# Performance work log

Measured on AMD Instinct MI355X. Metric: run time of the kernel, lower is better.

## Reference

```python
import jax, jax.numpy as jnp
import numpy as np
from jax import lax

# 4th-order Butterworth lowpass, scipy.signal.butter(4, 0.2)
B_COEF = np.array([0.004824343357716228, 0.019297373430864913, 0.02894606014629737,
                   0.019297373430864913, 0.004824343357716228], dtype=np.float32)
A_COEF = np.array([1.0, -2.369513007182038, 2.3139884144006453,
                   -1.0546654058785672, 0.18737949236818502], dtype=np.float32)


def setup_inputs() -> dict:
    key = jax.random.key(0)
    x = jax.random.normal(key, (8, 64, 48000), dtype=jnp.float32)
    return {"x": x, "b": jnp.asarray(B_COEF), "a": jnp.asarray(A_COEF)}


def _pad_odd(x, n):
    # Faithful to torch _pad_odd (including its exact slicing on the right side).
    left = 2.0 * x[..., 0:1] - jnp.flip(x[..., 0:n], axis=-1)
    right = 2.0 * x[..., -1:] - jnp.flip(x[..., -(n + 2):-2], axis=-1)
    return jnp.concatenate([left, x, right], axis=-1)


def _lfilter(x, a, b):
    # y[n] = (sum_k b[k] x[n-k] - sum_j a[j] y[n-j]) / a[0]
    a0 = a[0]
    bn = b / a0
    an = a[1:] / a0                      # [N], N = order
    ntaps = b.shape[0]                   # static
    N = a.shape[0] - 1                   # static
    T = x.shape[-1]
    # FIR part: small static tap loop, fully vectorized over batch/time.
    pad = [(0, 0)] * (x.ndim - 1) + [(ntaps - 1, 0)]
    xp = jnp.pad(x, pad)
    f = bn[0] * xp[..., ntaps - 1: ntaps - 1 + T]
    for k in range(1, ntaps):
        f = f + bn[k] * xp[..., ntaps - 1 - k: ntaps - 1 - k + T]
    # IIR recurrence via scan over time.
    f_t = jnp.moveaxis(f, -1, 0)         # [T, B, C]
    init = jnp.zeros(x.shape[:-1] + (N,), x.dtype)  # [B, C, N], y[t-1..t-N]

    def step(carry, ft):
        y = ft - jnp.einsum('k,...k->...', an, carry)
        carry = jnp.concatenate([y[..., None], carry[..., :-1]], axis=-1)
        return carry, y

    _, ys = lax.scan(step, init, f_t)
    return jnp.moveaxis(ys, 0, -1)       # [B, C, T]


def _filtfilt(x, a, b):
    y = _lfilter(x, a, b)
    return jnp.flip(_lfilter(jnp.flip(y, axis=-1), a, b), axis=-1)


def reference(x, b, a):
    scale = jnp.max(jnp.abs(x), axis=-1, keepdims=True)
    xs = x / scale
    padlen = 3 * max(int(a.shape[0]), int(b.shape[0]))  # 15, static
    xp = _pad_odd(xs, padlen)
    y = _filtfilt(xp, a, b)
    y = y[..., padlen:-padlen]
    return y * scale
```

## Files before the change

kernel.cpp:

```cpp
#include <hip/hip_runtime.h>


#define T48 48000
#define TP0 48030
#define LCH 48
#define NCH 1024
#define UF  8192

#define BAR_LDS() do { \
  asm volatile("s_waitcnt lgkmcnt(0)" ::: "memory"); \
  __builtin_amdgcn_s_barrier(); \
} while (0)

__device__ __forceinline__ float fget(const float4& v, int e) {
  switch (e & 3) { case 0: return v.x; case 1: return v.y; case 2: return v.z; default: return v.w; }
}

#define MAPPLY(t, M, q) do { \
  (t).x += (M)[0]*(q).x  + (M)[1]*(q).y  + (M)[2]*(q).z  + (M)[3]*(q).w; \
  (t).y += (M)[4]*(q).x  + (M)[5]*(q).y  + (M)[6]*(q).z  + (M)[7]*(q).w; \
  (t).z += (M)[8]*(q).x  + (M)[9]*(q).y  + (M)[10]*(q).z + (M)[11]*(q).w; \
  (t).w += (M)[12]*(q).x + (M)[13]*(q).y + (M)[14]*(q).z + (M)[15]*(q).w; \
} while (0)

__global__ __launch_bounds__(1024, 4) void filtfilt_k(
    const float* __restrict__ x, const float* __restrict__ bco,
    const float* __restrict__ aco, float* __restrict__ out)
{
  __shared__ __align__(16) float U[UF];
  __shared__ float P[3][16];

  const int c = threadIdx.x;
  const float* __restrict__ xs = x + (size_t)blockIdx.x * T48;
  const float4* __restrict__ xs4 = reinterpret_cast<const float4*>(xs);
  float* __restrict__ os = out + (size_t)blockIdx.x * T48;
  float4* __restrict__ os4 = reinterpret_cast<float4*>(os);
  float4* __restrict__ U4 = reinterpret_cast<float4*>(U);

  const float inva0 = 1.f / aco[0];
  const float b0 = bco[0]*inva0, b1 = bco[1]*inva0, b2 = bco[2]*inva0,
              b3 = bco[3]*inva0, b4 = bco[4]*inva0;
  const float na1 = -aco[1]*inva0, na2 = -aco[2]*inva0,
              na3 = -aco[3]*inva0, na4 = -aco[4]*inva0;

  float4 F[14];
  const int fb = 12*c - 5;
#pragma unroll
  for (int k = 0; k < 14; k++) {
    int m = min(max(fb + k, 0), 11999);
    F[k] = xs4[m];
  }

  if (c < 64) {
    const int i = (c >> 2) & 3, j = c & 3;
    float r1 = (j==0)?1.f:0.f, r2 = (j==1)?1.f:0.f,
          r3 = (j==2)?1.f:0.f, r4 = (j==3)?1.f:0.f;
#pragma unroll
    for (int n = 0; n < LCH; n++) {
      float h = fmaf(na1, r1, fmaf(na2, r2, fmaf(na3, r3, na4 * r4)));
      r4 = r3; r3 = r2; r2 = r1; r1 = h;
    }
    float c0 = __shfl(r1, j), c1 = __shfl(r2, j),
          c2 = __shfl(r3, j), c3 = __shfl(r4, j);
    float Pv = (i==0)?c0 : (i==1)?c1 : (i==2)?c2 : c3;
    if (c < 16) P[0][c] = Pv;
    const float P0v = Pv;
    {
      float rA0 = __shfl(Pv, i*4+0), rA1 = __shfl(Pv, i*4+1),
            rA2 = __shfl(Pv, i*4+2), rA3 = __shfl(Pv, i*4+3);
      float cB0 = __shfl(Pv, 0*4+j), cB1 = __shfl(Pv, 1*4+j),
            cB2 = __shfl(Pv, 2*4+j), cB3 = __shfl(Pv, 3*4+j);
      Pv = rA0*cB0 + rA1*cB1 + rA2*cB2 + rA3*cB3;
    }
    if (c < 16) P[1][c] = Pv;
    {
      float rA0 = __shfl(Pv, i*4+0), rA1 = __shfl(Pv, i*4+1),
            rA2 = __shfl(Pv, i*4+2), rA3 = __shfl(Pv, i*4+3);
      float cB0 = __shfl(P0v, 0*4+j), cB1 = __shfl(P0v, 1*4+j),
            cB2 = __shfl(P0v, 2*4+j), cB3 = __shfl(P0v, 3*4+j);
      Pv = rA0*cB0 + rA1*cB1 + rA2*cB2 + rA3*cB3;
    }
    if (c < 16) P[2][c] = Pv;
  }

  float w4v = F[0].y, w3v = F[0].z, w2v = F[0].w, w1v = F[1].x;
  float A[LCH];
#pragma unroll
  for (int n = 0; n < LCH; n++) A[n] = fget(F[(n + 5) >> 2], (n + 5) & 3);

  if (c == 0) {
    float x0d = 2.f * xs[0];
    w4v = 0.f; w3v = 0.f; w2v = 0.f; w1v = 0.f;
#pragma unroll
    for (int n = 0; n < 15; n++) A[n] = x0d - xs[14 - n];
  }
  if (c >= 1000) {
    float xld = 2.f * xs[T48 - 1];
#define RFIX(p, var) do { int _p = (p); \
    if (_p >= 48015) var = (_p < TP0) ? (xld - xs[96012 - _p]) : 0.f; } while (0)
    RFIX(48*c - 4, w4v); RFIX(48*c - 3, w3v);
    RFIX(48*c - 2, w2v); RFIX(48*c - 1, w1v);
#pragma unroll
    for (int n = 0; n < LCH; n++) {
      int p = 48*c + n;
      if (p >= 48015) A[n] = (p < TP0) ? (xld - xs[96012 - p]) : 0.f;
    }
#undef RFIX
  }

  BAR_LDS();

  float r1 = 0.f, r2 = 0.f, r3 = 0.f, r4 = 0.f;
#pragma unroll
  for (int n = 0; n < LCH; n++) {
    float xv = A[n];
    float f = fmaf(b0,xv, fmaf(b1,w1v, fmaf(b2,w2v, fmaf(b3,w3v, b4*w4v))));
    w4v = w3v; w3v = w2v; w2v = w1v; w1v = xv;
    float u = fmaf(na4, r4, f);
    u = fmaf(na3, r3, u); u = fmaf(na2, r2, u); u = fmaf(na1, r1, u);
    A[n] = u; r4 = r3; r3 = r2; r2 = r1; r1 = u;
  }

  float4* Sb0 = U4;
  float4* Sb1 = U4 + 1024;
  Sb0[c] = make_float4(r1, r2, r3, r4);
  BAR_LDS();
  float4 sv = make_float4(0.f,0.f,0.f,0.f);
  if (c > 0) {
    sv = Sb0[c-1];
    if (c > 1) { float4 q = Sb0[c-2]; MAPPLY(sv, P[0], q); }
    if (c > 2) { float4 q = Sb0[c-3]; MAPPLY(sv, P[1], q); }
    if (c > 3) { float4 q = Sb0[c-4]; MAPPLY(sv, P[2], q); }
  }

  {
    float h1 = sv.x, h2 = sv.y, h3 = sv.z, h4 = sv.w;
#pragma unroll
    for (int n = 0; n < LCH; n++) {
      float h = fmaf(na1, h1, fmaf(na2, h2, fmaf(na3, h3, na4 * h4)));
      A[n] += h;
      h4 = h3; h3 = h2; h2 = h1; h1 = h;
    }
  }
  if (c >= 1000) {
#pragma unroll
    for (int n = 0; n < LCH; n++) if (48*c + n >= TP0) A[n] = 0.f;
  }

  Sb1[c] = make_float4(A[0], A[1], A[2], A[3]);
  BAR_LDS();
  float h0 = 0.f, h1v = 0.f, h2v = 0.f, h3v = 0.f;
  if (c < NCH - 1) { float4 hv = Sb1[c+1]; h0 = hv.x; h1v = hv.y; h2v = hv.z; h3v = hv.w; }

#define YV(i) ((i) < 48 ? A[(i)] : ((i)==48 ? h0 : (i)==49 ? h1v : (i)==50 ? h2v : h3v))
  r1 = 0.f; r2 = 0.f; r3 = 0.f; r4 = 0.f;
#pragma unroll
  for (int m = 0; m < LCH; m++) {
    float g = fmaf(b0, YV(47-m), fmaf(b1, YV(48-m),
              fmaf(b2, YV(49-m), fmaf(b3, YV(50-m), b4 * YV(51-m)))));
    float u = fmaf(na4, r4, g);
    u = fmaf(na3, r3, u); u = fmaf(na2, r2, u); u = fmaf(na1, r1, u);
    r4 = r3; r3 = r2; r2 = r1; r1 = u;
    if      (m == 0) h3v = u;
    else if (m == 1) h2v = u;
    else if (m == 2) h1v = u;
    else if (m == 3) h0  = u;
    else             A[51 - m] = u;
  }
#undef YV

  const int d = NCH - 1 - c;
  Sb0[d] = make_float4(r1, r2, r3, r4);
  BAR_LDS();
  float4 ev = make_float4(0.f,0.f,0.f,0.f);
  if (d > 0) {
    ev = Sb0[d-1];
    if (d > 1) { float4 q = Sb0[d-2]; MAPPLY(ev, P[0], q); }
    if (d > 2) { float4 q = Sb0[d-3]; MAPPLY(ev, P[1], q); }
    if (d > 3) { float4 q = Sb0[d-4]; MAPPLY(ev, P[2], q); }
  }

  {
    float g1 = ev.x, g2 = ev.y, g3 = ev.z, g4 = ev.w;
#pragma unroll
    for (int m = 0; m < LCH; m++) {
      float h = fmaf(na1, g1, fmaf(na2, g2, fmaf(na3, g3, na4 * g4)));
      if      (m == 0) h3v += h;
      else if (m == 1) h2v += h;
      else if (m == 2) h1v += h;
      else if (m == 3) h0  += h;
      else             A[51 - m] += h;
      g4 = g3; g3 = g2; g2 = g1; g1 = h;
    }
  }

  {
    const int base = 48*c - 15;
    if (base >= 0 && base < T48 - 2) {
      os[base+0] = A[4]; os[base+1] = A[5]; os[base+2] = A[6];
    }
#pragma unroll
    for (int k = 0; k < 10; k++) {
      int t4 = 12*c - 3 + k;
      if (t4 >= 0 && t4 < 12000)
        os4[t4] = make_float4(A[7+4*k], A[8+4*k], A[9+4*k], A[10+4*k]);
    }
    {
      int t4 = 12*c + 7;
      if (t4 < 12000) os4[t4] = make_float4(A[47], h0, h1v, h2v);
    }
    {
      int t = 48*c + 32;
      if (t < T48) os[t] = h3v;
    }
  }
}

extern "C" void kernel_launch(void* const* d_in, const int* in_sizes, int n_in,
                              void* d_out, int out_size, void* d_ws, size_t ws_size,
                              hipStream_t stream) {
  (void)n_in; (void)d_ws; (void)ws_size; (void)out_size;
  const float* x = (const float*)d_in[0];
  const float* b = (const float*)d_in[1];
  const float* a = (const float*)d_in[2];
  float* out = (float*)d_out;
  const int nseq = in_sizes[0] / T48;
  filtfilt_k<<<dim3(nseq), dim3(1024), 0, stream>>>(x, b, a, out);
}
```

Baseline: 219.7 us.

## Split each sequence across four 256-thread blocks using truncated state propagation

Each sequence now goes to four 256-thread blocks instead of one 1024-thread block. Each block covers 251 output chunks plus two halo chunks, and the halo absorbs the chunk carry-ins. The inter-chunk state prefix is cut to two neighbour terms, dropping the precomputed P^2 and P^3 matrices, on the premise that the filter's impulse response decays to negligible size after about 96 samples. Output is staged through shared memory so each thread writes 12 aligned float4s, which removes the scalar and edge stores. This raises the block count and shrinks barrier scope, but it repeats the halo work and is only approximately exact because the recurrence is truncated.

New measurement: 199.1 us. -9.4%, faster.

```diff
diff --git a/kernel.cpp b/kernel.cpp
--- a/kernel.cpp
+++ b/kernel.cpp
@@ -4,8 +4,7 @@
 #define T48 48000
 #define TP0 48030
 #define LCH 48
-#define NCH 1024
-#define UF  8192
+#define NOUT 251
 
 #define BAR_LDS() do { \
   asm volatile("s_waitcnt lgkmcnt(0)" ::: "memory"); \
@@ -23,19 +22,21 @@
   (t).w += (M)[12]*(q).x + (M)[13]*(q).y + (M)[14]*(q).z + (M)[15]*(q).w; \
 } while (0)
 
-__global__ __launch_bounds__(1024, 4) void filtfilt_k(
+__global__ __launch_bounds__(256, 4) void filtfilt_k(
     const float* __restrict__ x, const float* __restrict__ bco,
     const float* __restrict__ aco, float* __restrict__ out)
 {
-  __shared__ __align__(16) float U[UF];
-  __shared__ float P[3][16];
-
-  const int c = threadIdx.x;
-  const float* __restrict__ xs = x + (size_t)blockIdx.x * T48;
+  __shared__ __align__(16) float4 S[1024];
+  __shared__ float P0s[16];
+
+  const int t   = threadIdx.x;
+  const int seq = blockIdx.x >> 2;
+  const int b   = blockIdx.x & 3;
+  const int gc  = NOUT*b - 2 + t;
+  const float* __restrict__ xs = x + (size_t)seq * T48;
   const float4* __restrict__ xs4 = reinterpret_cast<const float4*>(xs);
-  float* __restrict__ os = out + (size_t)blockIdx.x * T48;
+  float* __restrict__ os = out + (size_t)seq * T48;
   float4* __restrict__ os4 = reinterpret_cast<float4*>(os);
-  float4* __restrict__ U4 = reinterpret_cast<float4*>(U);
 
   const float inva0 = 1.f / aco[0];
   const float b0 = bco[0]*inva0, b1 = bco[1]*inva0, b2 = bco[2]*inva0,
@@ -44,15 +45,15 @@
               na3 = -aco[3]*inva0, na4 = -aco[4]*inva0;
 
   float4 F[14];
-  const int fb = 12*c - 5;
+  const int fb = 12*gc - 5;
 #pragma unroll
   for (int k = 0; k < 14; k++) {
     int m = min(max(fb + k, 0), 11999);
     F[k] = xs4[m];
   }
 
-  if (c < 64) {
-    const int i = (c >> 2) & 3, j = c & 3;
+  if (t < 64) {
+    const int i = (t >> 2) & 3, j = t & 3;
     float r1 = (j==0)?1.f:0.f, r2 = (j==1)?1.f:0.f,
           r3 = (j==2)?1.f:0.f, r4 = (j==3)?1.f:0.f;
 #pragma unroll
@@ -63,24 +64,7 @@
     float c0 = __shfl(r1, j), c1 = __shfl(r2, j),
           c2 = __shfl(r3, j), c3 = __shfl(r4, j);
     float Pv = (i==0)?c0 : (i==1)?c1 : (i==2)?c2 : c3;
-    if (c < 16) P[0][c] = Pv;
-    const float P0v = Pv;
-    {
-      float rA0 = __shfl(Pv, i*4+0), rA1 = __shfl(Pv, i*4+1),
-            rA2 = __shfl(Pv, i*4+2), rA3 = __shfl(Pv, i*4+3);
-      float cB0 = __shfl(Pv, 0*4+j), cB1 = __shfl(Pv, 1*4+j),
-            cB2 = __shfl(Pv, 2*4+j), cB3 = __shfl(Pv, 3*4+j);
-      Pv = rA0*cB0 + rA1*cB1 + rA2*cB2 + rA3*cB3;
-    }
-    if (c < 16) P[1][c] = Pv;
-    {
-      float rA0 = __shfl(Pv, i*4+0), rA1 = __shfl(Pv, i*4+1),
-            rA2 = __shfl(Pv, i*4+2), rA3 = __shfl(Pv, i*4+3);
-      float cB0 = __shfl(P0v, 0*4+j), cB1 = __shfl(P0v, 1*4+j),
-            cB2 = __shfl(P0v, 2*4+j), cB3 = __shfl(P0v, 3*4+j);
-      Pv = rA0*cB0 + rA1*cB1 + rA2*cB2 + rA3*cB3;
-    }
-    if (c < 16) P[2][c] = Pv;
+    if (t < 16) P0s[t] = Pv;
   }
 
   float w4v = F[0].y, w3v = F[0].z, w2v = F[0].w, w1v = F[1].x;
@@ -88,27 +72,29 @@
 #pragma unroll
   for (int n = 0; n < LCH; n++) A[n] = fget(F[(n + 5) >> 2], (n + 5) & 3);
 
-  if (c == 0) {
+  if (gc < 0) {
+    w4v = 0.f; w3v = 0.f; w2v = 0.f; w1v = 0.f;
+#pragma unroll
+    for (int n = 0; n < LCH; n++) A[n] = 0.f;
+  } else if (gc == 0) {
     float x0d = 2.f * xs[0];
     w4v = 0.f; w3v = 0.f; w2v = 0.f; w1v = 0.f;
 #pragma unroll
     for (int n = 0; n < 15; n++) A[n] = x0d - xs[14 - n];
   }
-  if (c >= 1000) {
+  if (gc >= 1000) {
     float xld = 2.f * xs[T48 - 1];
 #define RFIX(p, var) do { int _p = (p); \
     if (_p >= 48015) var = (_p < TP0) ? (xld - xs[96012 - _p]) : 0.f; } while (0)
-    RFIX(48*c - 4, w4v); RFIX(48*c - 3, w3v);
-    RFIX(48*c - 2, w2v); RFIX(48*c - 1, w1v);
+    RFIX(48*gc - 4, w4v); RFIX(48*gc - 3, w3v);
+    RFIX(48*gc - 2, w2v); RFIX(48*gc - 1, w1v);
 #pragma unroll
     for (int n = 0; n < LCH; n++) {
-      int p = 48*c + n;
+      int p = 48*gc + n;
       if (p >= 48015) A[n] = (p < TP0) ? (xld - xs[96012 - p]) : 0.f;
     }
 #undef RFIX
   }
-
-  BAR_LDS();
 
   float r1 = 0.f, r2 = 0.f, r3 = 0.f, r4 = 0.f;
 #pragma unroll
@@ -121,16 +107,13 @@
     A[n] = u; r4 = r3; r3 = r2; r2 = r1; r1 = u;
   }
 
-  float4* Sb0 = U4;
-  float4* Sb1 = U4 + 1024;
-  Sb0[c] = make_float4(r1, r2, r3, r4);
+  S[t] = make_float4(r1, r2, r3, r4);
   BAR_LDS();
   float4 sv = make_float4(0.f,0.f,0.f,0.f);
-  if (c > 0) {
-    sv = Sb0[c-1];
-    if (c > 1) { float4 q = Sb0[c-2]; MAPPLY(sv, P[0], q); }
-    if (c > 2) { float4 q = Sb0[c-3]; MAPPLY(sv, P[1], q); }
-    if (c > 3) { float4 q = Sb0[c-4]; MAPPLY(sv, P[2], q); }
+  if (t >= 2) {
+    sv = S[t-1];
+    float4 q = S[t-2];
+    MAPPLY(sv, P0s, q);
   }
 
   {
@@ -142,15 +125,15 @@
       h4 = h3; h3 = h2; h2 = h1; h1 = h;
     }
   }
-  if (c >= 1000) {
-#pragma unroll
-    for (int n = 0; n < LCH; n++) if (48*c + n >= TP0) A[n] = 0.f;
-  }
-
-  Sb1[c] = make_float4(A[0], A[1], A[2], A[3]);
+  if (gc >= 1000) {
+#pragma unroll
+    for (int n = 0; n < LCH; n++) if (48*gc + n >= TP0) A[n] = 0.f;
+  }
+
+  S[256 + t] = make_float4(A[0], A[1], A[2], A[3]);
   BAR_LDS();
   float h0 = 0.f, h1v = 0.f, h2v = 0.f, h3v = 0.f;
-  if (c < NCH - 1) { float4 hv = Sb1[c+1]; h0 = hv.x; h1v = hv.y; h2v = hv.z; h3v = hv.w; }
+  if (t < 255) { float4 hv = S[256 + t + 1]; h0 = hv.x; h1v = hv.y; h2v = hv.z; h3v = hv.w; }
 
 #define YV(i) ((i) < 48 ? A[(i)] : ((i)==48 ? h0 : (i)==49 ? h1v : (i)==50 ? h2v : h3v))
   r1 = 0.f; r2 = 0.f; r3 = 0.f; r4 = 0.f;
@@ -169,16 +152,14 @@
   }
 #undef YV
 
-  const int d = NCH - 1 - c;
-  Sb0[d] = make_float4(r1, r2, r3, r4);
+  S[512 + t] = make_float4(r1, r2, r3, r4);
   BAR_LDS();
   float4 ev = make_float4(0.f,0.f,0.f,0.f);
-  if (d > 0) {
-    ev = Sb0[d-1];
-    if (d > 1) { float4 q = Sb0[d-2]; MAPPLY(ev, P[0], q); }
-    if (d > 2) { float4 q = Sb0[d-3]; MAPPLY(ev, P[1], q); }
-    if (d > 3) { float4 q = Sb0[d-4]; MAPPLY(ev, P[2], q); }
-  }
+  if (t < 255) {
+    ev = S[512 + t + 1];
+    if (t < 254) { float4 q = S[512 + t + 2]; MAPPLY(ev, P0s, q); }
+  }
+  BAR_LDS();
 
   {
     float g1 = ev.x, g2 = ev.y, g3 = ev.z, g4 = ev.w;
@@ -194,25 +175,22 @@
     }
   }
 
-  {
-    const int base = 48*c - 15;
-    if (base >= 0 && base < T48 - 2) {
-      os[base+0] = A[4]; os[base+1] = A[5]; os[base+2] = A[6];
-    }
-#pragma unroll
-    for (int k = 0; k < 10; k++) {
-      int t4 = 12*c - 3 + k;
-      if (t4 >= 0 && t4 < 12000)
-        os4[t4] = make_float4(A[7+4*k], A[8+4*k], A[9+4*k], A[10+4*k]);
-    }
-    {
-      int t4 = 12*c + 7;
-      if (t4 < 12000) os4[t4] = make_float4(A[47], h0, h1v, h2v);
-    }
-    {
-      int t = 48*c + 32;
-      if (t < T48) os[t] = h3v;
-    }
+  S[4*t + 0] = make_float4(A[4],  A[5],  A[6],  A[7]);
+  S[4*t + 1] = make_float4(A[8],  A[9],  A[10], A[11]);
+  S[4*t + 2] = make_float4(A[12], A[13], A[14], A[15]);
+  S[4*t + 3] = make_float4(A[16], A[17], A[18], A[19]);
+  BAR_LDS();
+  if (t >= 2 && t < 253 && gc <= 999) {
+    float4 N0 = S[4*t + 4], N1 = S[4*t + 5], N2 = S[4*t + 6], N3 = S[4*t + 7];
+    float4* op = os4 + 12*gc;
+#pragma unroll
+    for (int k = 0; k < 7; k++)
+      op[k] = make_float4(A[19+4*k], A[20+4*k], A[21+4*k], A[22+4*k]);
+    op[7]  = make_float4(A[47], h0, h1v, h2v);
+    op[8]  = make_float4(h3v, N0.x, N0.y, N0.z);
+    op[9]  = make_float4(N0.w, N1.x, N1.y, N1.z);
+    op[10] = make_float4(N1.w, N2.x, N2.y, N2.z);
+    op[11] = make_float4(N2.w, N3.x, N3.y, N3.z);
   }
 }
 
@@ -225,5 +203,5 @@
   const float* a = (const float*)d_in[2];
   float* out = (float*)d_out;
   const int nseq = in_sizes[0] / T48;
-  filtfilt_k<<<dim3(nseq), dim3(1024), 0, stream>>>(x, b, a, out);
+  filtfilt_k<<<dim3(nseq * 4), dim3(256), 0, stream>>>(x, b, a, out);
 }
```
